# Kernel optimization log

Measured on AMD Instinct MI355X. Metric: run time of the kernel, lower is better.

Reference implementation:

```python
import jax, jax.numpy as jnp
import numpy as np

B, L, D_IN = 16, 2048, 512
HID, H = 512, 8
D = HID // H          # head dim
FACTOR = 5
U = min(FACTOR * int(np.ceil(np.log(L))), L)  # u_q == u_k == 40 (L == S)


def setup_inputs() -> dict:
    key = jax.random.key(0)
    ks = jax.random.split(key, 8)
    s = 1.0 / np.sqrt(D_IN).astype(np.float32)
    return {
        "q_in": jax.random.normal(ks[0], (B, L, D_IN), jnp.float32),
        "k_in": jax.random.normal(ks[1], (B, L, D_IN), jnp.float32),
        "v_in": jax.random.normal(ks[2], (B, L, D_IN), jnp.float32),
        "Wq": jax.random.normal(ks[3], (D_IN, HID), jnp.float32) * s,
        "Wk": jax.random.normal(ks[4], (D_IN, HID), jnp.float32) * s,
        "Wv": jax.random.normal(ks[5], (D_IN, HID), jnp.float32) * s,
        "Wo": jax.random.normal(ks[6], (HID, HID // H), jnp.float32) / np.sqrt(HID).astype(np.float32),
        "indx_q_seq": jax.random.randint(ks[7], (L,), 0, L, dtype=jnp.int32),
    }


def reference(q_in, k_in, v_in, Wq, Wk, Wv, Wo, indx_q_seq):
    # projections + (memory-reinterpreting, as in the TF source) head reshape
    q = (q_in @ Wq).reshape(B, H, L, D)
    k = (k_in @ Wk).reshape(B, H, L, D)
    v = (v_in @ Wv).reshape(B, H, L, D)

    # --- _prob_qk ---
    # TF's chained gathers on the broadcast k_expand collapse to pairing
    # query s with the single key indx_q_seq[s]; all sample_k columns of
    # Q_K_sample are identical, so M = max - sum/L = dot * (1 - U/L).
    k_sel = k[:, :, indx_q_seq, :]                        # [B,H,L,D]
    dot = jnp.einsum('bhle,bhle->bhl', q, k_sel)          # [B,H,L]
    M = dot - dot * (jnp.float32(U) / jnp.float32(L))
    _, m_top = jax.lax.top_k(M, U)                        # [B,H,U]

    b_idx = jnp.arange(B)[:, None, None]
    h_idx = jnp.arange(H)[None, :, None]
    q_red = q[b_idx, h_idx, m_top]                        # [B,H,U,D]
    scores = jnp.einsum('bhue,bhle->bhul', q_red, k)      # [B,H,U,L]
    scores = scores * (1.0 / np.sqrt(D).astype(np.float32))

    # --- initial context: causal cumsum of values ---
    context = jnp.cumsum(v, axis=-2)                      # [B,H,L,D]

    # --- update context at the top-U query positions (causal mask) ---
    causal = jnp.arange(L)[None, None, None, :] > m_top[..., None]
    scores = jnp.where(causal, -jnp.inf, scores)
    attn = jax.nn.softmax(scores, axis=-1)                # [B,H,U,L]
    upd = jnp.einsum('bhul,bhld->bhud', attn, v)          # [B,H,U,D]
    context = context.at[b_idx, h_idx, m_top].set(upd)

    out = context.reshape(B, L, HID) @ Wo                 # [B,L,HID//H]
    return out
```

## Files before the change

kernel.cpp:

```cpp
#include <hip/hip_runtime.h>
#include <hip/hip_bf16.h>
#include <math.h>

#define B_   16
#define L_   2048
#define DIN  512
#define HID_ 512
#define H_   8
#define D_   64
#define U_   40
#define BH   (B_*H_)

typedef unsigned short u16;
typedef unsigned int u32;
typedef unsigned long long u64;
typedef __bf16 bf16x8 __attribute__((ext_vector_type(8)));
typedef float f32x4 __attribute__((ext_vector_type(4)));

__device__ __forceinline__ u16 f2bf(float x) {
  __bf16 b = (__bf16)x;
  return __builtin_bit_cast(unsigned short, b);
}
__device__ __forceinline__ float bf2f(u16 h) {
  return __uint_as_float(((unsigned)h) << 16);
}
__device__ __forceinline__ float bflo(u32 x) { return __uint_as_float(x << 16); }
__device__ __forceinline__ float bfhi(u32 x) { return __uint_as_float(x & 0xFFFF0000u); }
__device__ __forceinline__ u32 pk2(float a, float b) {
  return (u32)f2bf(a) | ((u32)f2bf(b) << 16);
}
__device__ __forceinline__ void gload16(const u16* g, u16* l) {
  __builtin_amdgcn_global_load_lds(
      (__attribute__((address_space(1))) void*)(g),
      (__attribute__((address_space(3))) void*)(l), 16, 0, 0);
}
__device__ __forceinline__ u64 mkkey(float Mv, int l) {
  u32 fb = __float_as_uint(Mv);
  u32 mapped = (fb & 0x80000000u) ? ~fb : (fb | 0x80000000u);
  return ((u64)mapped << 32) | (u64)(0xFFFFFFFFu - (u32)l);
}

__global__ __launch_bounds__(256)
void wsplit_kernel(const float* __restrict__ W, u16* __restrict__ Bt) {
  int tid = blockIdx.x * 256 + threadIdx.x;
  int n = tid & 511, k = tid >> 9;
  float a = W[(size_t)k * 512 + n];
  u16 hi = f2bf(a);
  u16 lo = f2bf(a - bf2f(hi));
  int kb = k >> 5, kc = k & 31;
  int slotH = kc >> 3, wi = kc & 7;
  int swzH = (slotH     ^ (n & 7)) << 3;
  int swzL = ((4+slotH) ^ (n & 7)) << 3;
  Bt[(size_t)n * 1024 + kb * 64 + swzH + wi] = hi;
  Bt[(size_t)n * 1024 + kb * 64 + swzL + wi] = lo;
}

template<int NPASS>
__global__ __launch_bounds__(256, 4)
void gemm_proj(const float* __restrict__ A, const u16* __restrict__ Bt,
               float* __restrict__ C) {
  __shared__ u16 As[128 * 64];
  __shared__ u16 Bs[128 * 64];
  const int t = threadIdx.x;
  const int w = t >> 6, lane = t & 63;
  const int lhi = lane >> 4, l16 = lane & 15;
  const int row0 = blockIdx.x * 128, col0 = blockIdx.y * 128;
  const int wrow = (w >> 1) * 64, wcol = (w & 1) * 64;

  const u16* gB = Bt + (size_t)(col0 + w * 32 + (lane >> 3)) * 1024 + (lane & 7) * 8;
  u16* lB = &Bs[(w * 32) * 64];

  f32x4 acc[4][4];
  #pragma unroll
  for (int i = 0; i < 4; ++i)
    #pragma unroll
    for (int j = 0; j < 4; ++j) acc[i][j] = (f32x4){0.f, 0.f, 0.f, 0.f};

  for (int kb = 0; kb < 16; ++kb) {
    #pragma unroll
    for (int i = 0; i < 4; ++i)
      gload16(gB + kb * 64 + (size_t)i * 8 * 1024, lB + i * 8 * 64);
    #pragma unroll
    for (int i = 0; i < 4; ++i) {
      int r  = (t >> 3) + 32 * i;
      int c4 = (t & 7) * 4;
      float4 v = *reinterpret_cast<const float4*>(
          &A[(size_t)(row0 + r) * 512 + kb * 32 + c4]);
      ushort4 h4;
      h4.x = f2bf(v.x); h4.y = f2bf(v.y); h4.z = f2bf(v.z); h4.w = f2bf(v.w);
      int slotH = c4 >> 3, wi = c4 & 7;
      int baseH = r * 64 + (((slotH)     ^ (r & 7)) << 3) + wi;
      *reinterpret_cast<ushort4*>(&As[baseH]) = h4;
      if constexpr (NPASS == 3) {
        ushort4 lo4;
        lo4.x = f2bf(v.x - bf2f(h4.x)); lo4.y = f2bf(v.y - bf2f(h4.y));
        lo4.z = f2bf(v.z - bf2f(h4.z)); lo4.w = f2bf(v.w - bf2f(h4.w));
        int baseL = r * 64 + (((4 + slotH) ^ (r & 7)) << 3) + wi;
        *reinterpret_cast<ushort4*>(&As[baseL]) = lo4;
      }
    }
    __syncthreads();

    bf16x8 bfH[4], bfL[4];
    #pragma unroll
    for (int j = 0; j < 4; ++j) {
      int cb = wcol + j * 16 + l16;
      bfH[j] = *reinterpret_cast<const bf16x8*>(
          &Bs[cb * 64 + ((lhi ^ (cb & 7)) << 3)]);
      if constexpr (NPASS == 3)
        bfL[j] = *reinterpret_cast<const bf16x8*>(
            &Bs[cb * 64 + (((4 + lhi) ^ (cb & 7)) << 3)]);
    }
    #pragma unroll
    for (int i = 0; i < 4; ++i) {
      int ra = wrow + i * 16 + l16;
      bf16x8 aH = *reinterpret_cast<const bf16x8*>(
          &As[ra * 64 + ((lhi ^ (ra & 7)) << 3)]);
      #pragma unroll
      for (int j = 0; j < 4; ++j)
        acc[i][j] = __builtin_amdgcn_mfma_f32_16x16x32_bf16(aH, bfH[j], acc[i][j], 0, 0, 0);
      if constexpr (NPASS == 3) {
        bf16x8 aL = *reinterpret_cast<const bf16x8*>(
            &As[ra * 64 + (((4 + lhi) ^ (ra & 7)) << 3)]);
        #pragma unroll
        for (int j = 0; j < 4; ++j)
          acc[i][j] = __builtin_amdgcn_mfma_f32_16x16x32_bf16(aH, bfL[j], acc[i][j], 0, 0, 0);
        #pragma unroll
        for (int j = 0; j < 4; ++j)
          acc[i][j] = __builtin_amdgcn_mfma_f32_16x16x32_bf16(aL, bfH[j], acc[i][j], 0, 0, 0);
      }
    }
    __syncthreads();
  }
  #pragma unroll
  for (int i = 0; i < 4; ++i)
    #pragma unroll
    for (int j = 0; j < 4; ++j)
      #pragma unroll
      for (int r = 0; r < 4; ++r)
        C[(size_t)(row0 + wrow + i * 16 + lhi * 4 + r) * 512
          + col0 + wcol + j * 16 + l16] = acc[i][j][r];
}

__global__ __launch_bounds__(256)
void dotsel_kernel(const float* __restrict__ qp, const float* __restrict__ kp,
                   const int* __restrict__ indx, u64* __restrict__ cand) {
  __shared__ u64 keys[256];
  __shared__ u64 wmax[2][4];
  const int bh = blockIdx.x, ch = blockIdx.y;
  const int t = threadIdx.x, w = t >> 6, lane = t & 63;
  const size_t boff = (size_t)bh * 131072;
  const int l0 = ch * 256 + w * 64;
  const float cUL = 40.0f / 2048.0f;
  const int li = lane >> 4;
  const int dq = lane & 15;

  #pragma unroll 4
  for (int i = 0; i < 16; ++i) {
    int l = l0 + i * 4 + li;
    int ls = indx[l];
    float4 q4 = *reinterpret_cast<const float4*>(&qp[boff + (size_t)l * 64 + dq * 4]);
    float4 k4 = *reinterpret_cast<const float4*>(&kp[boff + (size_t)ls * 64 + dq * 4]);
    float p = q4.x * k4.x + q4.y * k4.y + q4.z * k4.z + q4.w * k4.w;
    p += __shfl_xor(p, 1, 64);
    p += __shfl_xor(p, 2, 64);
    p += __shfl_xor(p, 4, 64);
    p += __shfl_xor(p, 8, 64);
    if (dq == 0) {
      float Mv = p - p * cUL;
      keys[w * 64 + i * 4 + li] = mkkey(Mv, l);
    }
  }
  __syncthreads();

  u64 myk = keys[t];
  for (int u = 0; u < U_; ++u) {
    u64 b = myk;
    #pragma unroll
    for (int off = 32; off >= 1; off >>= 1) {
      u64 v = __shfl_xor(b, off, 64);
      if (v > b) b = v;
    }
    if (lane == 0) wmax[u & 1][w] = b;
    __syncthreads();
    const u64* wm = wmax[u & 1];
    u64 m = wm[0];
    if (wm[1] > m) m = wm[1];
    if (wm[2] > m) m = wm[2];
    if (wm[3] > m) m = wm[3];
    if (myk == m) myk = 0;
    if (t == 0) cand[((size_t)(bh * 8 + ch)) * U_ + u] = m;
  }
}

__global__ __launch_bounds__(64)
void merge_topk(const u64* __restrict__ cand, int* __restrict__ mtop) {
  const int bh = blockIdx.x;
  const int lane = threadIdx.x;
  u64 c0 = cand[(size_t)bh * 320 + 0 * 64 + lane];
  u64 c1 = cand[(size_t)bh * 320 + 1 * 64 + lane];
  u64 c2 = cand[(size_t)bh * 320 + 2 * 64 + lane];
  u64 c3 = cand[(size_t)bh * 320 + 3 * 64 + lane];
  u64 c4 = cand[(size_t)bh * 320 + 4 * 64 + lane];
  for (int u = 0; u < U_; ++u) {
    u64 b = c0;
    if (c1 > b) b = c1;
    if (c2 > b) b = c2;
    if (c3 > b) b = c3;
    if (c4 > b) b = c4;
    #pragma unroll
    for (int off = 32; off >= 1; off >>= 1) {
      u64 v = __shfl_xor(b, off, 64);
      if (v > b) b = v;
    }
    if (c0 == b) c0 = 0;
    if (c1 == b) c1 = 0;
    if (c2 == b) c2 = 0;
    if (c3 == b) c3 = 0;
    if (c4 == b) c4 = 0;
    if (lane == 0) mtop[bh * U_ + u] = (int)(0xFFFFFFFFu - (u32)b);
  }
}

__global__ __launch_bounds__(256)
void gather_q_kernel(const float* __restrict__ qp, const int* __restrict__ mtop,
                     u16* __restrict__ qredbf) {
  int tid = blockIdx.x * 256 + threadIdx.x;
  int s = tid >> 6;
  int d = tid & 63;
  int bh = s / 48;
  int u = s - bh * 48;
  float val = 0.f;
  if (u < U_) {
    int m = mtop[bh * U_ + u];
    val = qp[(size_t)bh * (L_ * D_) + (size_t)m * D_ + d] * 0.125f;
  }
  qredbf[tid] = f2bf(val);
}

__global__ __launch_bounds__(256)
void scores_mfma(const u16* __restrict__ qredbf, const float* __restrict__ kp,
                 const int* __restrict__ mtop, u16* __restrict__ S) {
  __shared__ u16 As[48 * 64];
  __shared__ u16 Bs[128 * 64];
  __shared__ int ms[U_];
  const int bh = blockIdx.x;
  const int l0 = blockIdx.y * 128;
  const int t = threadIdx.x, w = t >> 6, lane = t & 63;
  const int lhi = lane >> 4, l16 = lane & 15;

  for (int e = t; e < 384; e += 256) {
    int r = e >> 3, s = e & 7;
    *reinterpret_cast<uint4*>(&As[r * 64 + ((s ^ (r & 7)) << 3)]) =
        *reinterpret_cast<const uint4*>(&qredbf[(size_t)bh * 3072 + e * 8]);
  }
  #pragma unroll
  for (int ee = 0; ee < 4; ++ee) {
    int e = t + ee * 256;
    int r = e >> 3, s = e & 7;
    const float* src = &kp[(size_t)bh * 131072 + (size_t)(l0 + r) * 64 + s * 8];
    float4 va = *reinterpret_cast<const float4*>(src);
    float4 vb = *reinterpret_cast<const float4*>(src + 4);
    uint4 w4 = make_uint4(pk2(va.x, va.y), pk2(va.z, va.w),
                          pk2(vb.x, vb.y), pk2(vb.z, vb.w));
    *reinterpret_cast<uint4*>(&Bs[r * 64 + ((s ^ (r & 7)) << 3)]) = w4;
  }
  if (t < U_) ms[t] = mtop[bh * U_ + t];
  __syncthreads();

  f32x4 acc[3][2];
  #pragma unroll
  for (int m = 0; m < 3; ++m)
    #pragma unroll
    for (int n = 0; n < 2; ++n) acc[m][n] = (f32x4){0.f, 0.f, 0.f, 0.f};

  #pragma unroll
  for (int ks = 0; ks < 2; ++ks) {
    bf16x8 a[3], b[2];
    #pragma unroll
    for (int m = 0; m < 3; ++m) {
      int r = m * 16 + l16;
      a[m] = *reinterpret_cast<const bf16x8*>(
          &As[r * 64 + (((ks * 4 + lhi) ^ (r & 7)) << 3)]);
    }
    #pragma unroll
    for (int n = 0; n < 2; ++n) {
      int cb = w * 32 + n * 16 + l16;
      b[n] = *reinterpret_cast<const bf16x8*>(
          &Bs[cb * 64 + (((ks * 4 + lhi) ^ (cb & 7)) << 3)]);
    }
    #pragma unroll
    for (int m = 0; m < 3; ++m)
      #pragma unroll
      for (int n = 0; n < 2; ++n)
        acc[m][n] = __builtin_amdgcn_mfma_f32_16x16x32_bf16(a[m], b[n], acc[m][n], 0, 0, 0);
  }

  #pragma unroll
  for (int m = 0; m < 3; ++m)
    #pragma unroll
    for (int n = 0; n < 2; ++n)
      #pragma unroll
      for (int r = 0; r < 4; ++r) {
        int u = m * 16 + lhi * 4 + r;
        if (u < U_) {
          int l = l0 + w * 32 + n * 16 + l16;
          float val = acc[m][n][r];
          if (l > ms[u]) val = -INFINITY;
          S[((size_t)bh * 48 + u) * 2048 + l] = f2bf(val);
        }
      }
}

__global__ __launch_bounds__(256)
void softmax_kernel(u16* __restrict__ S) {
  __shared__ float red[4];
  const int rr = blockIdx.x;
  const int bh = rr / U_;
  const int u = rr - bh * U_;
  const int t = threadIdx.x;
  uint4* rp = reinterpret_cast<uint4*>(&S[((size_t)bh * 48 + u) * 2048]);
  uint4 raw = rp[t];
  float f[8];
  f[0] = bflo(raw.x); f[1] = bfhi(raw.x); f[2] = bflo(raw.y); f[3] = bfhi(raw.y);
  f[4] = bflo(raw.z); f[5] = bfhi(raw.z); f[6] = bflo(raw.w); f[7] = bfhi(raw.w);
  float m = f[0];
  #pragma unroll
  for (int i = 1; i < 8; ++i) m = fmaxf(m, f[i]);
  #pragma unroll
  for (int off = 32; off >= 1; off >>= 1) m = fmaxf(m, __shfl_xor(m, off, 64));
  if ((t & 63) == 0) red[t >> 6] = m;
  __syncthreads();
  m = fmaxf(fmaxf(red[0], red[1]), fmaxf(red[2], red[3]));
  __syncthreads();
  float s = 0.f;
  #pragma unroll
  for (int i = 0; i < 8; ++i) { f[i] = expf(f[i] - m); s += f[i]; }
  #pragma unroll
  for (int off = 32; off >= 1; off >>= 1) s += __shfl_xor(s, off, 64);
  if ((t & 63) == 0) red[t >> 6] = s;
  __syncthreads();
  s = red[0] + red[1] + red[2] + red[3];
  float inv = 1.0f / s;
  uint4 o;
  o.x = pk2(f[0] * inv, f[1] * inv);
  o.y = pk2(f[2] * inv, f[3] * inv);
  o.z = pk2(f[4] * inv, f[5] * inv);
  o.w = pk2(f[6] * inv, f[7] * inv);
  rp[t] = o;
}

__global__ __launch_bounds__(256)
void pv_mfma(const u16* __restrict__ Pbf, const float* __restrict__ vp,
             float* __restrict__ partial) {
  __shared__ u16 Ps[48 * 128];
  __shared__ u16 Vs[64 * 128];
  const int bh = blockIdx.x, kh = blockIdx.y;
  const int t = threadIdx.x, w = t >> 6, lane = t & 63;
  const int lhi = lane >> 4, l16 = lane & 15;
  const size_t vbase = (size_t)bh * 131072;
  f32x4 acc[3];
  #pragma unroll
  for (int m = 0; m < 3; ++m) acc[m] = (f32x4){0.f, 0.f, 0.f, 0.f};

  for (int ch = 0; ch < 2; ++ch) {
    const int lb = kh * 256 + ch * 128;
    for (int e = t; e < 768; e += 256) {
      int r = e >> 4, s = e & 15;
      int sw = (s & 8) | ((s & 7) ^ (r & 7));
      *reinterpret_cast<uint4*>(&Ps[r * 128 + (sw << 3)]) =
          *reinterpret_cast<const uint4*>(&Pbf[((size_t)bh * 48 + r) * 2048 + lb + s * 8]);
    }
    #pragma unroll
    for (int j = 0; j < 16; ++j) {
      int ll = w * 32 + 2 * j;
      float a = vp[vbase + (size_t)(lb + ll) * 64 + lane];
      float b = vp[vbase + (size_t)(lb + ll + 1) * 64 + lane];
      u32 pk = pk2(a, b);
      int s = ll >> 3;
      int sw = (s & 8) | ((s & 7) ^ (lane & 7));
      *reinterpret_cast<u32*>(&Vs[lane * 128 + (sw << 3) + (ll & 7)]) = pk;
    }
    __syncthreads();
    #pragma unroll
    for (int ks = 0; ks < 4; ++ks) {
      bf16x8 b;
      { int cb = w * 16 + l16; int s = ks * 4 + lhi;
        int sw = (s & 8) | ((s & 7) ^ (cb & 7));
        b = *reinterpret_cast<const bf16x8*>(&Vs[cb * 128 + (sw << 3)]); }
      #pragma unroll
      for (int m = 0; m < 3; ++m) {
        int r = m * 16 + l16; int s = ks * 4 + lhi;
        int sw = (s & 8) | ((s & 7) ^ (r & 7));
        bf16x8 a = *reinterpret_cast<const bf16x8*>(&Ps[r * 128 + (sw << 3)]);
        acc[m] = __builtin_amdgcn_mfma_f32_16x16x32_bf16(a, b, acc[m], 0, 0, 0);
      }
    }
    __syncthreads();
  }
  #pragma unroll
  for (int m = 0; m < 3; ++m)
    #pragma unroll
    for (int r = 0; r < 4; ++r) {
      int u = m * 16 + lhi * 4 + r;
      partial[(((size_t)kh * 128 + bh) * 48 + u) * 64 + w * 16 + l16] = acc[m][r];
    }
}

__global__ __launch_bounds__(256)
void cumsumA(const float* __restrict__ vp, float* __restrict__ seg32) {
  int bh = blockIdx.x, sg = blockIdx.y;
  int t = threadIdx.x, w = t >> 6, lane = t & 63;
  int g = sg * 4 + w;
  size_t base = (size_t)bh * 131072 + (size_t)g * 32 * 64;
  float s = 0.f;
  for (int i = 0; i < 32; ++i) s += vp[base + i * 64 + lane];
  seg32[((size_t)bh * 64 + g) * 64 + lane] = s;
}
__global__ __launch_bounds__(256)
void cumsumB(const float* __restrict__ vp, const float* __restrict__ seg32,
             float* __restrict__ ctx) {
  int bh = blockIdx.x, sg = blockIdx.y;
  int t = threadIdx.x, w = t >> 6, lane = t & 63;
  int g = sg * 4 + w;
  float run = 0.f;
  for (int s = 0; s < g; ++s) run += seg32[((size_t)bh * 64 + s) * 64 + lane];
  size_t base = (size_t)bh * 131072 + (size_t)g * 32 * 64;
  for (int i = 0; i < 32; ++i) {
    run += vp[base + i * 64 + lane];
    ctx[base + i * 64 + lane] = run;
  }
}

__global__ __launch_bounds__(256)
void scatter_kernel(const float* __restrict__ partial, const int* __restrict__ mtop,
                    float* __restrict__ ctx) {
  int tid = blockIdx.x * 256 + threadIdx.x;
  int s = tid >> 6;
  if (s >= BH * U_) return;
  int d = tid & 63;
  int bh = s / U_;
  int u = s - bh * U_;
  float a = 0.f;
  #pragma unroll
  for (int c = 0; c < 8; ++c)
    a += partial[(((size_t)(c * 128 + bh)) * 48 + u) * 64 + d];
  ctx[(size_t)bh * 131072 + (size_t)mtop[s] * 64 + d] = a;
}

__global__ __launch_bounds__(256)
void wo_prep(const float* __restrict__ Wo, u16* __restrict__ WoT) {
  int tid = blockIdx.x * 256 + threadIdx.x;
  int j = tid >> 9, k = tid & 511;
  float v = Wo[(size_t)k * 64 + j];
  int k0 = k & ~63, ko = k & 63;
  int ks = ko >> 5, kc = ko & 31;
  int slot = (ks * 4 + (kc >> 3)) ^ (j & 7);
  WoT[(size_t)j * 512 + k0 + (slot << 3) + (kc & 7)] = f2bf(v);
}

__global__ __launch_bounds__(256, 6)
void gemm_out(const float* __restrict__ ctx, const u16* __restrict__ WoT,
              float* __restrict__ out) {
  __shared__ u16 As[64 * 64];
  __shared__ u16 Bs[64 * 64];
  const int t = threadIdx.x, w = t >> 6, lane = t & 63;
  const int lhi = lane >> 4, l16 = lane & 15;
  const int row0 = blockIdx.x * 64;
  f32x4 acc[4];
  #pragma unroll
  for (int j = 0; j < 4; ++j) acc[j] = (f32x4){0.f, 0.f, 0.f, 0.f};

  for (int k0 = 0; k0 < 512; k0 += 64) {
    #pragma unroll
    for (int ii = 0; ii < 2; ++ii) {
      int e = t + ii * 256;
      int j = e >> 3, s = e & 7;
      gload16(WoT + (size_t)j * 512 + k0 + s * 8, Bs + (size_t)(w * 64 + ii * 256) * 8);
    }
    #pragma unroll
    for (int ii = 0; ii < 2; ++ii) {
      int e = t + ii * 256;
      int r = e >> 3, s = e & 7;
      const float* src = &ctx[(size_t)(row0 + r) * 512 + k0 + s * 8];
      float4 va = *reinterpret_cast<const float4*>(src);
      float4 vb = *reinterpret_cast<const float4*>(src + 4);
      uint4 w4 = make_uint4(pk2(va.x, va.y), pk2(va.z, va.w),
                            pk2(vb.x, vb.y), pk2(vb.z, vb.w));
      *reinterpret_cast<uint4*>(&As[r * 64 + ((s ^ (r & 7)) << 3)]) = w4;
    }
    __syncthreads();
    #pragma unroll
    for (int ks = 0; ks < 2; ++ks) {
      int r = w * 16 + l16;
      bf16x8 a = *reinterpret_cast<const bf16x8*>(
          &As[r * 64 + (((ks * 4 + lhi) ^ (r & 7)) << 3)]);
      #pragma unroll
      for (int jf = 0; jf < 4; ++jf) {
        int cb = jf * 16 + l16;
        bf16x8 b = *reinterpret_cast<const bf16x8*>(
            &Bs[cb * 64 + (((ks * 4 + lhi) ^ (cb & 7)) << 3)]);
        acc[jf] = __builtin_amdgcn_mfma_f32_16x16x32_bf16(a, b, acc[jf], 0, 0, 0);
      }
    }
    __syncthreads();
  }
  #pragma unroll
  for (int jf = 0; jf < 4; ++jf)
    #pragma unroll
    for (int r = 0; r < 4; ++r)
      out[(size_t)(row0 + w * 16 + lhi * 4 + r) * 64 + jf * 16 + l16] = acc[jf][r];
}

extern "C" void kernel_launch(void* const* d_in, const int* in_sizes, int n_in,
                              void* d_out, int out_size, void* d_ws, size_t ws_size,
                              hipStream_t stream) {
  const float* q_in = (const float*)d_in[0];
  const float* k_in = (const float*)d_in[1];
  const float* v_in = (const float*)d_in[2];
  const float* Wq   = (const float*)d_in[3];
  const float* Wk   = (const float*)d_in[4];
  const float* Wv   = (const float*)d_in[5];
  const float* Wo   = (const float*)d_in[6];
  const int*   indx = (const int*)d_in[7];
  float* out = (float*)d_out;

  float* ws = (float*)d_ws;
  float* qp   = ws;
  float* kp   = ws + 16777216;
  float* vp   = ws + 33554432;
  u16*   Bt   = (u16*)(ws + 50331648);
  u64*   cand = (u64*)Bt;
  u16*   WoT  = (u16*)Bt;
  u16*   qredbf = (u16*)(ws + 50593792);
  int*   mtop = (int*)(ws + 50921472);
  u16*   S    = (u16*)qp;
  float* ctx  = qp;
  float* partial = kp;
  float* seg32   = kp + 3145728;

  const int M = B_ * L_;

  wsplit_kernel<<<1024, 256, 0, stream>>>(Wq, Bt);
  gemm_proj<3><<<dim3(M / 128, 4), 256, 0, stream>>>(q_in, Bt, qp);
  wsplit_kernel<<<1024, 256, 0, stream>>>(Wk, Bt);
  gemm_proj<3><<<dim3(M / 128, 4), 256, 0, stream>>>(k_in, Bt, kp);
  wsplit_kernel<<<1024, 256, 0, stream>>>(Wv, Bt);
  gemm_proj<1><<<dim3(M / 128, 4), 256, 0, stream>>>(v_in, Bt, vp);

  dotsel_kernel<<<dim3(BH, 8), 256, 0, stream>>>(qp, kp, indx, cand);
  merge_topk<<<BH, 64, 0, stream>>>(cand, mtop);
  gather_q_kernel<<<(BH * 48 * 64) / 256, 256, 0, stream>>>(qp, mtop, qredbf);

  scores_mfma<<<dim3(BH, 16), 256, 0, stream>>>(qredbf, kp, mtop, S);
  softmax_kernel<<<BH * U_, 256, 0, stream>>>(S);
  pv_mfma<<<dim3(BH, 8), 256, 0, stream>>>(S, vp, partial);

  cumsumA<<<dim3(BH, 16), 256, 0, stream>>>(vp, seg32);
  cumsumB<<<dim3(BH, 16), 256, 0, stream>>>(vp, seg32, ctx);

  scatter_kernel<<<(BH * U_ * 64) / 256, 256, 0, stream>>>(partial, mtop, ctx);

  wo_prep<<<128, 256, 0, stream>>>(Wo, WoT);
  gemm_out<<<M / 64, 256, 0, stream>>>(ctx, WoT, out);
}
```

Baseline: 364.6 us.

## Double-buffer projection GEMM, batch Q/K projections, store V as bf16

The projection GEMM now double-buffers B tiles in LDS and prefetches A directly into registers, converting to bf16 fragments in-register rather than staging A through shared memory. The Q and K projections run in one launch via blockIdx.z, and the three weight splits are fused into one kernel that uses the output buffer as scratch. V's projection is written as bf16, which halves the traffic for the pv and cumsum readers. The cost is higher register pressure (occupancy hint lowered to 3) and cumsum accumulating from bf16-rounded V values.

```diff
diff --git a/kernel.cpp b/kernel.cpp
--- a/kernel.cpp
+++ b/kernel.cpp
@@ -41,7 +41,10 @@
 }
 
 __global__ __launch_bounds__(256)
-void wsplit_kernel(const float* __restrict__ W, u16* __restrict__ Bt) {
+void wsplit3_kernel(const float* __restrict__ Wq, const float* __restrict__ Wk,
+                    const float* __restrict__ Wv, u16* __restrict__ Bt3) {
+  const float* W = (blockIdx.y == 0) ? Wq : (blockIdx.y == 1) ? Wk : Wv;
+  u16* Bt = Bt3 + (size_t)blockIdx.y * 524288;
   int tid = blockIdx.x * 256 + threadIdx.x;
   int n = tid & 511, k = tid >> 9;
   float a = W[(size_t)k * 512 + n];
@@ -55,12 +58,15 @@
   Bt[(size_t)n * 1024 + kb * 64 + swzL + wi] = lo;
 }
 
-template<int NPASS>
-__global__ __launch_bounds__(256, 4)
-void gemm_proj(const float* __restrict__ A, const u16* __restrict__ Bt,
-               float* __restrict__ C) {
-  __shared__ u16 As[128 * 64];
-  __shared__ u16 Bs[128 * 64];
+template<int NPASS, int OUTBF>
+__global__ __launch_bounds__(256, 3)
+void gemm_proj(const float* __restrict__ A0, const float* __restrict__ A1,
+               const u16* __restrict__ Bt0, const u16* __restrict__ Bt1,
+               void* __restrict__ C0, void* __restrict__ C1) {
+  __shared__ u16 Bs[2 * 128 * 64];
+  const float* A = blockIdx.z ? A1 : A0;
+  const u16* Bt  = blockIdx.z ? Bt1 : Bt0;
+  void* C        = blockIdx.z ? C1 : C0;
   const int t = threadIdx.x;
   const int w = t >> 6, lane = t & 63;
   const int lhi = lane >> 4, l16 = lane & 15;
@@ -68,7 +74,7 @@
   const int wrow = (w >> 1) * 64, wcol = (w & 1) * 64;
 
   const u16* gB = Bt + (size_t)(col0 + w * 32 + (lane >> 3)) * 1024 + (lane & 7) * 8;
-  u16* lB = &Bs[(w * 32) * 64];
+  const float* Abase = A + (size_t)(row0 + wrow + l16) * 512 + lhi * 8;
 
   f32x4 acc[4][4];
   #pragma unroll
@@ -76,70 +82,84 @@
     #pragma unroll
     for (int j = 0; j < 4; ++j) acc[i][j] = (f32x4){0.f, 0.f, 0.f, 0.f};
 
-  for (int kb = 0; kb < 16; ++kb) {
-    #pragma unroll
-    for (int i = 0; i < 4; ++i)
-      gload16(gB + kb * 64 + (size_t)i * 8 * 1024, lB + i * 8 * 64);
-    #pragma unroll
-    for (int i = 0; i < 4; ++i) {
-      int r  = (t >> 3) + 32 * i;
-      int c4 = (t & 7) * 4;
-      float4 v = *reinterpret_cast<const float4*>(
-          &A[(size_t)(row0 + r) * 512 + kb * 32 + c4]);
-      ushort4 h4;
-      h4.x = f2bf(v.x); h4.y = f2bf(v.y); h4.z = f2bf(v.z); h4.w = f2bf(v.w);
-      int slotH = c4 >> 3, wi = c4 & 7;
-      int baseH = r * 64 + (((slotH)     ^ (r & 7)) << 3) + wi;
-      *reinterpret_cast<ushort4*>(&As[baseH]) = h4;
-      if constexpr (NPASS == 3) {
-        ushort4 lo4;
-        lo4.x = f2bf(v.x - bf2f(h4.x)); lo4.y = f2bf(v.y - bf2f(h4.y));
-        lo4.z = f2bf(v.z - bf2f(h4.z)); lo4.w = f2bf(v.w - bf2f(h4.w));
-        int baseL = r * 64 + (((4 + slotH) ^ (r & 7)) << 3) + wi;
-        *reinterpret_cast<ushort4*>(&As[baseL]) = lo4;
-      }
-    }
-    __syncthreads();
-
-    bf16x8 bfH[4], bfL[4];
-    #pragma unroll
-    for (int j = 0; j < 4; ++j) {
-      int cb = wcol + j * 16 + l16;
-      bfH[j] = *reinterpret_cast<const bf16x8*>(
-          &Bs[cb * 64 + ((lhi ^ (cb & 7)) << 3)]);
-      if constexpr (NPASS == 3)
-        bfL[j] = *reinterpret_cast<const bf16x8*>(
-            &Bs[cb * 64 + (((4 + lhi) ^ (cb & 7)) << 3)]);
-    }
-    #pragma unroll
-    for (int i = 0; i < 4; ++i) {
-      int ra = wrow + i * 16 + l16;
-      bf16x8 aH = *reinterpret_cast<const bf16x8*>(
-          &As[ra * 64 + ((lhi ^ (ra & 7)) << 3)]);
-      #pragma unroll
-      for (int j = 0; j < 4; ++j)
-        acc[i][j] = __builtin_amdgcn_mfma_f32_16x16x32_bf16(aH, bfH[j], acc[i][j], 0, 0, 0);
-      if constexpr (NPASS == 3) {
-        bf16x8 aL = *reinterpret_cast<const bf16x8*>(
-            &As[ra * 64 + (((4 + lhi) ^ (ra & 7)) << 3)]);
-        #pragma unroll
-        for (int j = 0; j < 4; ++j)
-          acc[i][j] = __builtin_amdgcn_mfma_f32_16x16x32_bf16(aH, bfL[j], acc[i][j], 0, 0, 0);
-        #pragma unroll
-        for (int j = 0; j < 4; ++j)
-          acc[i][j] = __builtin_amdgcn_mfma_f32_16x16x32_bf16(aL, bfH[j], acc[i][j], 0, 0, 0);
-      }
-    }
-    __syncthreads();
-  }
+  float4 ra[8], rb[8];
+  bf16x8 aH[4], aL[4];
+
+#define STAGEB(KB, NB)                                                          \
+  { u16* lB = &Bs[(NB) * 8192 + (w * 32) * 64];                                 \
+    _Pragma("unroll") for (int i = 0; i < 4; ++i)                               \
+      gload16(gB + (KB) * 64 + (size_t)i * 8 * 1024, lB + i * 8 * 64); }
+
+#define LOADA(DST, KB)                                                          \
+  { _Pragma("unroll") for (int i = 0; i < 4; ++i) {                             \
+      const float4* pa = reinterpret_cast<const float4*>(                       \
+          Abase + (size_t)i * 16 * 512 + (KB) * 32);                            \
+      DST[2*i] = pa[0]; DST[2*i+1] = pa[1]; } }
+
+#define CVTA(SRC)                                                               \
+  { _Pragma("unroll") for (int i = 0; i < 4; ++i) {                             \
+      float4 x = SRC[2*i], y = SRC[2*i+1];                                      \
+      aH[i][0]=(__bf16)x.x; aH[i][1]=(__bf16)x.y; aH[i][2]=(__bf16)x.z;         \
+      aH[i][3]=(__bf16)x.w; aH[i][4]=(__bf16)y.x; aH[i][5]=(__bf16)y.y;         \
+      aH[i][6]=(__bf16)y.z; aH[i][7]=(__bf16)y.w;                               \
+      if constexpr (NPASS == 3) {                                               \
+        aL[i][0]=(__bf16)(x.x-(float)aH[i][0]); aL[i][1]=(__bf16)(x.y-(float)aH[i][1]); \
+        aL[i][2]=(__bf16)(x.z-(float)aH[i][2]); aL[i][3]=(__bf16)(x.w-(float)aH[i][3]); \
+        aL[i][4]=(__bf16)(y.x-(float)aH[i][4]); aL[i][5]=(__bf16)(y.y-(float)aH[i][5]); \
+        aL[i][6]=(__bf16)(y.z-(float)aH[i][6]); aL[i][7]=(__bf16)(y.w-(float)aH[i][7]); } } }
+
+#define MFMAP(NB)                                                               \
+  { bf16x8 bH[4];                                                               \
+    _Pragma("unroll") for (int j = 0; j < 4; ++j) {                             \
+      int cb = wcol + j * 16 + l16;                                             \
+      bH[j] = *reinterpret_cast<const bf16x8*>(                                 \
+          &Bs[(NB) * 8192 + cb * 64 + ((lhi ^ (cb & 7)) << 3)]); }              \
+    _Pragma("unroll") for (int i = 0; i < 4; ++i)                               \
+      _Pragma("unroll") for (int j = 0; j < 4; ++j)                             \
+        acc[i][j] = __builtin_amdgcn_mfma_f32_16x16x32_bf16(aH[i], bH[j], acc[i][j], 0, 0, 0); \
+    if constexpr (NPASS == 3) {                                                 \
+      _Pragma("unroll") for (int j = 0; j < 4; ++j) {                           \
+        int cb = wcol + j * 16 + l16;                                           \
+        bf16x8 bL = *reinterpret_cast<const bf16x8*>(                           \
+            &Bs[(NB) * 8192 + cb * 64 + (((4 + lhi) ^ (cb & 7)) << 3)]);        \
+        _Pragma("unroll") for (int i = 0; i < 4; ++i)                           \
+          acc[i][j] = __builtin_amdgcn_mfma_f32_16x16x32_bf16(aH[i], bL, acc[i][j], 0, 0, 0); } \
+      _Pragma("unroll") for (int i = 0; i < 4; ++i)                             \
+        _Pragma("unroll") for (int j = 0; j < 4; ++j)                           \
+          acc[i][j] = __builtin_amdgcn_mfma_f32_16x16x32_bf16(aL[i], bH[j], acc[i][j], 0, 0, 0); } }
+
+#define STEP(KB, CUR, NXT)                                                      \
+  { if ((KB) < 15) { STAGEB((KB)+1, ((KB)+1)&1); LOADA(NXT, (KB)+1); }          \
+    CVTA(CUR);                                                                  \
+    MFMAP((KB)&1);                                                              \
+    __syncthreads(); }
+
+  STAGEB(0, 0)
+  LOADA(ra, 0)
+  __syncthreads();
+
+  STEP(0, ra, rb)  STEP(1, rb, ra)  STEP(2, ra, rb)  STEP(3, rb, ra)
+  STEP(4, ra, rb)  STEP(5, rb, ra)  STEP(6, ra, rb)  STEP(7, rb, ra)
+  STEP(8, ra, rb)  STEP(9, rb, ra)  STEP(10, ra, rb) STEP(11, rb, ra)
+  STEP(12, ra, rb) STEP(13, rb, ra) STEP(14, ra, rb) STEP(15, rb, ra)
+
+#undef STEP
+#undef MFMAP
+#undef CVTA
+#undef LOADA
+#undef STAGEB
+
   #pragma unroll
   for (int i = 0; i < 4; ++i)
     #pragma unroll
     for (int j = 0; j < 4; ++j)
       #pragma unroll
-      for (int r = 0; r < 4; ++r)
-        C[(size_t)(row0 + wrow + i * 16 + lhi * 4 + r) * 512
-          + col0 + wcol + j * 16 + l16] = acc[i][j][r];
+      for (int r = 0; r < 4; ++r) {
+        size_t idx = (size_t)(row0 + wrow + i * 16 + lhi * 4 + r) * 512
+                     + col0 + wcol + j * 16 + l16;
+        if constexpr (OUTBF) ((u16*)C)[idx] = f2bf(acc[i][j][r]);
+        else                 ((float*)C)[idx] = acc[i][j][r];
+      }
 }
 
 __global__ __launch_bounds__(256)
@@ -351,7 +371,7 @@
 }
 
 __global__ __launch_bounds__(256)
-void pv_mfma(const u16* __restrict__ Pbf, const float* __restrict__ vp,
+void pv_mfma(const u16* __restrict__ Pbf, const u16* __restrict__ vbf,
              float* __restrict__ partial) {
   __shared__ u16 Ps[48 * 128];
   __shared__ u16 Vs[64 * 128];
@@ -374,9 +394,9 @@
     #pragma unroll
     for (int j = 0; j < 16; ++j) {
       int ll = w * 32 + 2 * j;
-      float a = vp[vbase + (size_t)(lb + ll) * 64 + lane];
-      float b = vp[vbase + (size_t)(lb + ll + 1) * 64 + lane];
-      u32 pk = pk2(a, b);
+      u16 ua = vbf[vbase + (size_t)(lb + ll) * 64 + lane];
+      u16 ub = vbf[vbase + (size_t)(lb + ll + 1) * 64 + lane];
+      u32 pk = (u32)ua | ((u32)ub << 16);
       int s = ll >> 3;
       int sw = (s & 8) | ((s & 7) ^ (lane & 7));
       *reinterpret_cast<u32*>(&Vs[lane * 128 + (sw << 3) + (ll & 7)]) = pk;
@@ -408,17 +428,17 @@
 }
 
 __global__ __launch_bounds__(256)
-void cumsumA(const float* __restrict__ vp, float* __restrict__ seg32) {
+void cumsumA(const u16* __restrict__ vbf, float* __restrict__ seg32) {
   int bh = blockIdx.x, sg = blockIdx.y;
   int t = threadIdx.x, w = t >> 6, lane = t & 63;
   int g = sg * 4 + w;
   size_t base = (size_t)bh * 131072 + (size_t)g * 32 * 64;
   float s = 0.f;
-  for (int i = 0; i < 32; ++i) s += vp[base + i * 64 + lane];
+  for (int i = 0; i < 32; ++i) s += bf2f(vbf[base + i * 64 + lane]);
   seg32[((size_t)bh * 64 + g) * 64 + lane] = s;
 }
 __global__ __launch_bounds__(256)
-void cumsumB(const float* __restrict__ vp, const float* __restrict__ seg32,
+void cumsumB(const u16* __restrict__ vbf, const float* __restrict__ seg32,
              float* __restrict__ ctx) {
   int bh = blockIdx.x, sg = blockIdx.y;
   int t = threadIdx.x, w = t >> 6, lane = t & 63;
@@ -427,7 +447,7 @@
   for (int s = 0; s < g; ++s) run += seg32[((size_t)bh * 64 + s) * 64 + lane];
   size_t base = (size_t)bh * 131072 + (size_t)g * 32 * 64;
   for (int i = 0; i < 32; ++i) {
-    run += vp[base + i * 64 + lane];
+    run += bf2f(vbf[base + i * 64 + lane]);
     ctx[base + i * 64 + lane] = run;
   }
 }
@@ -528,12 +548,12 @@
   float* ws = (float*)d_ws;
   float* qp   = ws;
   float* kp   = ws + 16777216;
-  float* vp   = ws + 33554432;
-  u16*   Bt   = (u16*)(ws + 50331648);
-  u64*   cand = (u64*)Bt;
-  u16*   WoT  = (u16*)Bt;
+  u16*   vbf  = (u16*)(ws + 33554432);
+  u64*   cand = (u64*)(ws + 50331648);
+  u16*   WoT  = (u16*)cand;
   u16*   qredbf = (u16*)(ws + 50593792);
   int*   mtop = (int*)(ws + 50921472);
+  u16*   Bt3  = (u16*)d_out;
   u16*   S    = (u16*)qp;
   float* ctx  = qp;
   float* partial = kp;
@@ -541,12 +561,12 @@
 
   const int M = B_ * L_;
 
-  wsplit_kernel<<<1024, 256, 0, stream>>>(Wq, Bt);
-  gemm_proj<3><<<dim3(M / 128, 4), 256, 0, stream>>>(q_in, Bt, qp);
-  wsplit_kernel<<<1024, 256, 0, stream>>>(Wk, Bt);
-  gemm_proj<3><<<dim3(M / 128, 4), 256, 0, stream>>>(k_in, Bt, kp);
-  wsplit_kernel<<<1024, 256, 0, stream>>>(Wv, Bt);
-  gemm_proj<1><<<dim3(M / 128, 4), 256, 0, stream>>>(v_in, Bt, vp);
+  wsplit3_kernel<<<dim3(1024, 3), 256, 0, stream>>>(Wq, Wk, Wv, Bt3);
+
+  gemm_proj<3, 0><<<dim3(M / 128, 4, 2), 256, 0, stream>>>(
+      q_in, k_in, Bt3, Bt3 + 524288, qp, kp);
+  gemm_proj<1, 1><<<dim3(M / 128, 4, 1), 256, 0, stream>>>(
+      v_in, v_in, Bt3 + 1048576, Bt3 + 1048576, vbf, vbf);
 
   dotsel_kernel<<<dim3(BH, 8), 256, 0, stream>>>(qp, kp, indx, cand);
   merge_topk<<<BH, 64, 0, stream>>>(cand, mtop);
@@ -554,10 +574,10 @@
 
   scores_mfma<<<dim3(BH, 16), 256, 0, stream>>>(qredbf, kp, mtop, S);
   softmax_kernel<<<BH * U_, 256, 0, stream>>>(S);
-  pv_mfma<<<dim3(BH, 8), 256, 0, stream>>>(S, vp, partial);
-
-  cumsumA<<<dim3(BH, 16), 256, 0, stream>>>(vp, seg32);
-  cumsumB<<<dim3(BH, 16), 256, 0, stream>>>(vp, seg32, ctx);
+  pv_mfma<<<dim3(BH, 8), 256, 0, stream>>>(S, vbf, partial);
+
+  cumsumA<<<dim3(BH, 16), 256, 0, stream>>>(vbf, seg32);
+  cumsumB<<<dim3(BH, 16), 256, 0, stream>>>(vbf, seg32, ctx);
 
   scatter_kernel<<<(BH * U_ * 64) / 256, 256, 0, stream>>>(partial, mtop, ctx);
 
```

Result: slower. 421.6 us (+15.6%).

## Store V projection as bf16, batch weight splits, and swizzle GEMM block order

Applied to the files above, without the earlier changes.

The V projection now writes bf16 instead of fp32, and pv_mfma and the cumsum kernels read those bf16 values. This roughly halves V write and read traffic. The three weight-split kernels become one launch writing into the output buffer as scratch. The projection GEMM maps a 1D grid to tiles in groups of 8 row blocks times 4 column blocks for better L2 reuse of A. The cumulative sum now accumulates bf16-rounded V values, which adds rounding error to the context.

```diff
diff --git a/kernel.cpp b/kernel.cpp
--- a/kernel.cpp
+++ b/kernel.cpp
@@ -41,7 +41,10 @@
 }
 
 __global__ __launch_bounds__(256)
-void wsplit_kernel(const float* __restrict__ W, u16* __restrict__ Bt) {
+void wsplit3_kernel(const float* __restrict__ Wq, const float* __restrict__ Wk,
+                    const float* __restrict__ Wv, u16* __restrict__ Bt3) {
+  const float* W = (blockIdx.y == 0) ? Wq : (blockIdx.y == 1) ? Wk : Wv;
+  u16* Bt = Bt3 + (size_t)blockIdx.y * 524288;
   int tid = blockIdx.x * 256 + threadIdx.x;
   int n = tid & 511, k = tid >> 9;
   float a = W[(size_t)k * 512 + n];
@@ -55,16 +58,20 @@
   Bt[(size_t)n * 1024 + kb * 64 + swzL + wi] = lo;
 }
 
-template<int NPASS>
+template<int NPASS, int OUTBF>
 __global__ __launch_bounds__(256, 4)
 void gemm_proj(const float* __restrict__ A, const u16* __restrict__ Bt,
-               float* __restrict__ C) {
+               void* __restrict__ C) {
   __shared__ u16 As[128 * 64];
   __shared__ u16 Bs[128 * 64];
+  const int bid = blockIdx.x;
+  const int g = bid >> 3;
+  const int xb = (bid & 7) + ((g >> 2) << 3);
+  const int yb = g & 3;
   const int t = threadIdx.x;
   const int w = t >> 6, lane = t & 63;
   const int lhi = lane >> 4, l16 = lane & 15;
-  const int row0 = blockIdx.x * 128, col0 = blockIdx.y * 128;
+  const int row0 = xb * 128, col0 = yb * 128;
   const int wrow = (w >> 1) * 64, wcol = (w & 1) * 64;
 
   const u16* gB = Bt + (size_t)(col0 + w * 32 + (lane >> 3)) * 1024 + (lane & 7) * 8;
@@ -137,9 +144,12 @@
     #pragma unroll
     for (int j = 0; j < 4; ++j)
       #pragma unroll
-      for (int r = 0; r < 4; ++r)
-        C[(size_t)(row0 + wrow + i * 16 + lhi * 4 + r) * 512
-          + col0 + wcol + j * 16 + l16] = acc[i][j][r];
+      for (int r = 0; r < 4; ++r) {
+        size_t idx = (size_t)(row0 + wrow + i * 16 + lhi * 4 + r) * 512
+                     + col0 + wcol + j * 16 + l16;
+        if constexpr (OUTBF) ((u16*)C)[idx] = f2bf(acc[i][j][r]);
+        else                 ((float*)C)[idx] = acc[i][j][r];
+      }
 }
 
 __global__ __launch_bounds__(256)
@@ -351,7 +361,7 @@
 }
 
 __global__ __launch_bounds__(256)
-void pv_mfma(const u16* __restrict__ Pbf, const float* __restrict__ vp,
+void pv_mfma(const u16* __restrict__ Pbf, const u16* __restrict__ vbf,
              float* __restrict__ partial) {
   __shared__ u16 Ps[48 * 128];
   __shared__ u16 Vs[64 * 128];
@@ -374,9 +384,9 @@
     #pragma unroll
     for (int j = 0; j < 16; ++j) {
       int ll = w * 32 + 2 * j;
-      float a = vp[vbase + (size_t)(lb + ll) * 64 + lane];
-      float b = vp[vbase + (size_t)(lb + ll + 1) * 64 + lane];
-      u32 pk = pk2(a, b);
+      u16 ua = vbf[vbase + (size_t)(lb + ll) * 64 + lane];
+      u16 ub = vbf[vbase + (size_t)(lb + ll + 1) * 64 + lane];
+      u32 pk = (u32)ua | ((u32)ub << 16);
       int s = ll >> 3;
       int sw = (s & 8) | ((s & 7) ^ (lane & 7));
       *reinterpret_cast<u32*>(&Vs[lane * 128 + (sw << 3) + (ll & 7)]) = pk;
@@ -408,17 +418,17 @@
 }
 
 __global__ __launch_bounds__(256)
-void cumsumA(const float* __restrict__ vp, float* __restrict__ seg32) {
+void cumsumA(const u16* __restrict__ vbf, float* __restrict__ seg32) {
   int bh = blockIdx.x, sg = blockIdx.y;
   int t = threadIdx.x, w = t >> 6, lane = t & 63;
   int g = sg * 4 + w;
   size_t base = (size_t)bh * 131072 + (size_t)g * 32 * 64;
   float s = 0.f;
-  for (int i = 0; i < 32; ++i) s += vp[base + i * 64 + lane];
+  for (int i = 0; i < 32; ++i) s += bf2f(vbf[base + i * 64 + lane]);
   seg32[((size_t)bh * 64 + g) * 64 + lane] = s;
 }
 __global__ __launch_bounds__(256)
-void cumsumB(const float* __restrict__ vp, const float* __restrict__ seg32,
+void cumsumB(const u16* __restrict__ vbf, const float* __restrict__ seg32,
              float* __restrict__ ctx) {
   int bh = blockIdx.x, sg = blockIdx.y;
   int t = threadIdx.x, w = t >> 6, lane = t & 63;
@@ -427,7 +437,7 @@
   for (int s = 0; s < g; ++s) run += seg32[((size_t)bh * 64 + s) * 64 + lane];
   size_t base = (size_t)bh * 131072 + (size_t)g * 32 * 64;
   for (int i = 0; i < 32; ++i) {
-    run += vp[base + i * 64 + lane];
+    run += bf2f(vbf[base + i * 64 + lane]);
     ctx[base + i * 64 + lane] = run;
   }
 }
@@ -528,12 +538,12 @@
   float* ws = (float*)d_ws;
   float* qp   = ws;
   float* kp   = ws + 16777216;
-  float* vp   = ws + 33554432;
-  u16*   Bt   = (u16*)(ws + 50331648);
-  u64*   cand = (u64*)Bt;
-  u16*   WoT  = (u16*)Bt;
+  u16*   vbf  = (u16*)(ws + 33554432);
+  u64*   cand = (u64*)(ws + 50331648);
+  u16*   WoT  = (u16*)cand;
   u16*   qredbf = (u16*)(ws + 50593792);
   int*   mtop = (int*)(ws + 50921472);
+  u16*   Bt3  = (u16*)d_out;
   u16*   S    = (u16*)qp;
   float* ctx  = qp;
   float* partial = kp;
@@ -541,12 +551,11 @@
 
   const int M = B_ * L_;
 
-  wsplit_kernel<<<1024, 256, 0, stream>>>(Wq, Bt);
-  gemm_proj<3><<<dim3(M / 128, 4), 256, 0, stream>>>(q_in, Bt, qp);
-  wsplit_kernel<<<1024, 256, 0, stream>>>(Wk, Bt);
-  gemm_proj<3><<<dim3(M / 128, 4), 256, 0, stream>>>(k_in, Bt, kp);
-  wsplit_kernel<<<1024, 256, 0, stream>>>(Wv, Bt);
-  gemm_proj<1><<<dim3(M / 128, 4), 256, 0, stream>>>(v_in, Bt, vp);
+  wsplit3_kernel<<<dim3(1024, 3), 256, 0, stream>>>(Wq, Wk, Wv, Bt3);
+
+  gemm_proj<3, 0><<<1024, 256, 0, stream>>>(q_in, Bt3, qp);
+  gemm_proj<3, 0><<<1024, 256, 0, stream>>>(k_in, Bt3 + 524288, kp);
+  gemm_proj<1, 1><<<1024, 256, 0, stream>>>(v_in, Bt3 + 1048576, vbf);
 
   dotsel_kernel<<<dim3(BH, 8), 256, 0, stream>>>(qp, kp, indx, cand);
   merge_topk<<<BH, 64, 0, stream>>>(cand, mtop);
@@ -554,10 +563,10 @@
 
   scores_mfma<<<dim3(BH, 16), 256, 0, stream>>>(qredbf, kp, mtop, S);
   softmax_kernel<<<BH * U_, 256, 0, stream>>>(S);
-  pv_mfma<<<dim3(BH, 8), 256, 0, stream>>>(S, vp, partial);
-
-  cumsumA<<<dim3(BH, 16), 256, 0, stream>>>(vp, seg32);
-  cumsumB<<<dim3(BH, 16), 256, 0, stream>>>(vp, seg32, ctx);
+  pv_mfma<<<dim3(BH, 8), 256, 0, stream>>>(S, vbf, partial);
+
+  cumsumA<<<dim3(BH, 16), 256, 0, stream>>>(vbf, seg32);
+  cumsumB<<<dim3(BH, 16), 256, 0, stream>>>(vbf, seg32, ctx);
 
   scatter_kernel<<<(BH * U_ * 64) / 256, 256, 0, stream>>>(partial, mtop, ctx);
 
```

Result: faster. 337.8 us (-7.4%).
